# Performance work log

Measured on AMD Instinct MI355X. Metric: run time of the kernel, lower is better.

The kernel has to match this reference:

```python
import jax, jax.numpy as jnp
import numpy as np

EPS = 1e-5
RADIUS = 1.0

def bn(x, gamma, beta, axis=1):
    # inference-mode BatchNorm1d: running_mean=0, running_var=1
    shape = [1] * x.ndim
    shape[axis] = -1
    return x * (gamma / jnp.sqrt(1.0 + EPS)).reshape(shape) + beta.reshape(shape)

def pconv(x, w):
    # pointwise Conv1d (kernel_size=1): x [B,Cin,N], w [Cout,Cin]
    return jnp.einsum('oi,bin->bon', w, x)

def sq_dist(a, b):
    # a [B,N,3], b [B,S,3] -> squared pairwise distances [B,N,S]
    return (jnp.sum(a * a, -1)[:, :, None] + jnp.sum(b * b, -1)[:, None, :]
            - 2.0 * jnp.einsum('bnc,bsc->bns', a, b))

def index_points(points, idx):
    # points [B,S,...], idx [B,...] -> gathered [B, idx.shape[1:], ...]
    return jax.vmap(lambda p, i: p[i])(points, idx)

def fps(xyz, npoint):
    # farthest point sampling (deterministic start at index 0)
    B, N, _ = xyz.shape
    binds = jnp.arange(B)
    def step(carry, _):
        dist, far = carry
        c = xyz[binds, far]                                    # [B,3]
        d = jnp.sum((xyz - c[:, None, :]) ** 2, -1)            # [B,N]
        dist = jnp.minimum(dist, d)
        nxt = jnp.argmax(dist, -1).astype(jnp.int32)
        return (dist, nxt), far
    init = (jnp.full((B, N), 1e10, xyz.dtype), jnp.zeros((B,), jnp.int32))
    _, idx = jax.lax.scan(step, init, None, length=npoint)
    return jnp.transpose(idx)                                   # [B,npoint]

def query_ball(radius, nsample, xyz, new_xyz):
    # indices of first nsample points within radius of each center
    B, N, _ = xyz.shape
    S = new_xyz.shape[1]
    d2 = sq_dist(new_xyz, xyz)                                  # [B,S,N]
    gidx = jnp.broadcast_to(jnp.arange(N, dtype=jnp.int32), (B, S, N))
    gidx = jnp.where(d2 > radius * radius, N, gidx)
    gidx = jnp.sort(gidx, axis=-1)[:, :, :nsample]
    first = gidx[:, :, :1]
    gidx = jnp.where(gidx == N, first, gidx)
    return jnp.clip(gidx, 0, N - 1)

def sample_and_group(npoint, nsample, radius, xyz, points):
    fps_idx = fps(xyz, npoint)
    new_xyz = index_points(xyz, fps_idx)                        # [B,S,3]
    new_pts = index_points(points, fps_idx)                     # [B,S,D]
    idx = query_ball(radius, nsample, xyz, new_xyz)             # [B,S,K]
    grouped = index_points(points, idx)                         # [B,S,K,D]
    centered = grouped - new_pts[:, :, None, :]
    rep = jnp.broadcast_to(new_pts[:, :, None, :], centered.shape)
    return new_xyz, jnp.concatenate([centered, rep], axis=-1)   # [B,S,K,2D]

def local_op(x, w1, g1, b1, w2, g2, b2):
    # x [B,n,K,d]; shared pointwise MLP over channels then max over K
    h = jnp.einsum('oi,bnki->bnok', w1, x)
    h = jax.nn.relu(bn(h, g1, b1, axis=2))
    h = jnp.einsum('oi,bnik->bnok', w2, h)
    h = jax.nn.relu(bn(h, g2, b2, axis=2))
    return jnp.transpose(jnp.max(h, -1), (0, 2, 1))             # [B,out,n]

def feature_prop(xyz1, xyz2, points1, points2, w1, g1, b1, w2, g2, b2):
    # 3-NN inverse-distance interpolation of points2 onto xyz1, concat points1
    p1 = jnp.transpose(xyz1, (0, 2, 1))                         # [B,N,3]
    p2 = jnp.transpose(xyz2, (0, 2, 1))                         # [B,S,3]
    f2 = jnp.transpose(points2, (0, 2, 1))                      # [B,S,D2]
    negd, idx = jax.lax.top_k(-sq_dist(p1, p2), 3)              # [B,N,3]
    recip = 1.0 / (-negd + 1e-8)
    w = recip / jnp.sum(recip, -1, keepdims=True)
    interp = jnp.sum(index_points(f2, idx) * w[..., None], 2)   # [B,N,D2]
    new = jnp.concatenate([points1, jnp.transpose(interp, (0, 2, 1))], axis=1)
    new = jax.nn.relu(bn(pconv(new, w1), g1, b1))
    new = jax.nn.relu(bn(pconv(new, w2), g2, b2))
    return new


def setup_inputs() -> dict:
    key = jax.random.key(0)
    ks = iter(jax.random.split(key, 80))
    def W(*s):  return jax.random.normal(next(ks), s, jnp.float32) * 0.05
    def G(n):   return 1.0 + 0.1 * jax.random.normal(next(ks), (n,), jnp.float32)
    def Bt(n):  return 0.1 * jax.random.normal(next(ks), (n,), jnp.float32)
    inp = {"x": jax.random.uniform(next(ks), (4, 8192, 3), jnp.float32)}
    inp.update(w_emb1=W(64, 3), g_emb1=G(64), be_emb1=Bt(64),
               w_emb2=W(64, 64), g_emb2=G(64), be_emb2=Bt(64),
               l0_w1=W(128, 128), l0_g1=G(128), l0_b1=Bt(128),
               l0_w2=W(128, 128), l0_g2=G(128), l0_b2=Bt(128),
               l1_w1=W(256, 256), l1_g1=G(256), l1_b1=Bt(256),
               l1_w2=W(256, 256), l1_g2=G(256), l1_b2=Bt(256),
               f0_w1=W(256, 384), f0_g1=G(256), f0_b1=Bt(256),
               f0_w2=W(512, 256), f0_g2=G(512), f0_b2=Bt(512),
               f1_w1=W(512, 576), f1_g1=G(512), f1_b1=Bt(512),
               f1_w2=W(1024, 512), f1_g2=G(1024), f1_b2=Bt(1024),
               c1_w=W(512, 1024), c1_bias=Bt(512), c1_g=G(512), c1_beta=Bt(512),
               c2_w=W(128, 512), c2_bias=Bt(128), c2_g=G(128), c2_beta=Bt(128),
               out_w=W(8, 128), out_bias=Bt(8))
    return inp


def reference(x, w_emb1, g_emb1, be_emb1, w_emb2, g_emb2, be_emb2,
              l0_w1, l0_g1, l0_b1, l0_w2, l0_g2, l0_b2,
              l1_w1, l1_g1, l1_b1, l1_w2, l1_g2, l1_b2,
              f0_w1, f0_g1, f0_b1, f0_w2, f0_g2, f0_b2,
              f1_w1, f1_g1, f1_b1, f1_w2, f1_g2, f1_b2,
              c1_w, c1_bias, c1_g, c1_beta, c2_w, c2_bias, c2_g, c2_beta,
              out_w, out_bias):
    xyz = x                                                     # [B,N,3]
    h = jnp.transpose(x, (0, 2, 1))                             # [B,3,N]
    h = jax.nn.relu(bn(pconv(h, w_emb1), g_emb1, be_emb1))
    h = jax.nn.relu(bn(pconv(h, w_emb2), g_emb2, be_emb2))
    feats0 = h                                                  # [B,64,N]
    xyz1, g1f = sample_and_group(2048, 32, RADIUS, xyz, jnp.transpose(h, (0, 2, 1)))
    feats1 = local_op(g1f, l0_w1, l0_g1, l0_b1, l0_w2, l0_g2, l0_b2)   # [B,128,2048]
    xyz2, g2f = sample_and_group(1024, 32, RADIUS, xyz1, jnp.transpose(feats1, (0, 2, 1)))
    feats2 = local_op(g2f, l1_w1, l1_g1, l1_b1, l1_w2, l1_g2, l1_b2)   # [B,256,1024]
    h = feature_prop(jnp.transpose(xyz1, (0, 2, 1)), jnp.transpose(xyz2, (0, 2, 1)),
                     feats1, feats2, f0_w1, f0_g1, f0_b1, f0_w2, f0_g2, f0_b2)   # [B,512,2048]
    h = feature_prop(jnp.transpose(xyz, (0, 2, 1)), jnp.transpose(xyz1, (0, 2, 1)),
                     feats0, h, f1_w1, f1_g1, f1_b1, f1_w2, f1_g2, f1_b2)        # [B,1024,N]
    h = jax.nn.relu(bn(pconv(h, c1_w) + c1_bias[None, :, None], c1_g, c1_beta))
    h = jax.nn.relu(bn(pconv(h, c2_w) + c2_bias[None, :, None], c2_g, c2_beta))
    logits = pconv(h, out_w) + out_bias[None, :, None]
    return jnp.transpose(logits, (0, 2, 1))                     # [B,N,labels]
```

## Files before the change

### kernel.cpp

```cpp
#include <hip/hip_runtime.h>
#include <math.h>


static constexpr size_t O_FEATS0 = 0;
static constexpr size_t O_FEATS1 = 8388608;
static constexpr size_t O_FEATS2 = 12582912;
static constexpr size_t O_FP0OUT = 16777216;
static constexpr size_t O_XYZ1   = 33554432;
static constexpr size_t O_XYZ2   = 33652736;
static constexpr size_t O_FPS1   = 33701888;
static constexpr size_t O_FPS2   = 33734656;
static constexpr size_t O_BALL1  = 33751040;
static constexpr size_t O_BALL2  = 34799616;
static constexpr size_t O_NN0I   = 35323904;
static constexpr size_t O_NN0W   = 35422208;
static constexpr size_t O_NN1I   = 35520512;
static constexpr size_t O_NN1W   = 35913728;
static constexpr size_t O_REG0   = 36306944;
static constexpr size_t O_REG1   = 103415808;
static constexpr size_t WS_NEED  = 170524672;

typedef float v2f __attribute__((ext_vector_type(2)));

__device__ __forceinline__ unsigned long long u64max(unsigned long long a,
                                                     unsigned long long b) {
  return a > b ? a : b;
}
template <int CTRL>
__device__ __forceinline__ unsigned long long dpp_step(unsigned long long k) {
  const int lo = (int)(unsigned)k;
  const int hi = (int)(unsigned)(k >> 32);
  const int nlo = __builtin_amdgcn_update_dpp(lo, lo, CTRL, 0xf, 0xf, false);
  const int nhi = __builtin_amdgcn_update_dpp(hi, hi, CTRL, 0xf, 0xf, false);
  return ((unsigned long long)(unsigned)nhi << 32) | (unsigned)nlo;
}

template <int N, int NP, bool EMB>
__global__ __launch_bounds__(256, 1) void fps_kernel(
    const float* __restrict__ xyz, int* __restrict__ out,
    float* __restrict__ oxyz, const float* __restrict__ w1,
    const float* __restrict__ g1, const float* __restrict__ b1,
    const float* __restrict__ w2, const float* __restrict__ g2,
    const float* __restrict__ b2, float* __restrict__ femb) {
  #pragma clang fp contract(off)
  constexpr int PPT = N / 256;
  constexpr int PAIRS = PPT / 2;
  __shared__ float sx[N], sy[N], sz[N];
  __shared__ int sfar[NP];
  __shared__ unsigned long long skey[2][4];

  if constexpr (EMB) {
    if (blockIdx.x >= 4) {
      #pragma clang fp contract(fast)
      const int bid = blockIdx.x - 4;
      const int t = threadIdx.x;
      const int o = t & 63, pl = t >> 6;
      const int pt = bid * 4 + pl;
      const float x0 = xyz[(size_t)pt * 3 + 0];
      const float x1 = xyz[(size_t)pt * 3 + 1];
      const float x2 = xyz[(size_t)pt * 3 + 2];
      const float SQ = sqrtf(1.0f + 1e-5f);
      float v = w1[o * 3 + 0] * x0 + w1[o * 3 + 1] * x1 + w1[o * 3 + 2] * x2;
      v = fmaxf(v * (g1[o] / SQ) + b1[o], 0.0f);
      float* h = sx;
      h[pl * 64 + o] = v;
      __syncthreads();
      float acc = 0.0f;
      #pragma unroll 8
      for (int i = 0; i < 64; ++i) acc += w2[o * 64 + i] * h[pl * 64 + i];
      float y = fmaxf(acc * (g2[o] / SQ) + b2[o], 0.0f);
      femb[(size_t)pt * 64 + o] = y;
      return;
    }
  }

  const int b = blockIdx.x, t = threadIdx.x;
  const float* xb = xyz + (size_t)b * N * 3;
  for (int i = t; i < N; i += 256) {
    sx[i] = xb[i * 3 + 0];
    sy[i] = xb[i * 3 + 1];
    sz[i] = xb[i * 3 + 2];
  }
  __syncthreads();
  v2f px[PAIRS], py[PAIRS], pz[PAIRS], ds[PAIRS];
  #pragma unroll
  for (int k = 0; k < PAIRS; ++k) {
    const int g = t * PPT + 2 * k;
    px[k].x = sx[g]; px[k].y = sx[g + 1];
    py[k].x = sy[g]; py[k].y = sy[g + 1];
    pz[k].x = sz[g]; pz[k].y = sz[g + 1];
    ds[k].x = 1e10f; ds[k].y = 1e10f;
  }
  const int wid = t >> 6, lane = t & 63;
  int far = 0;
  float ccx = sx[0], ccy = sy[0], ccz = sz[0];
  for (int it = 0; it < NP; ++it) {
    if (t == 0) sfar[it] = far;
    v2f cx2, cy2, cz2;
    cx2.x = ccx; cx2.y = ccx;
    cy2.x = ccy; cy2.y = ccy;
    cz2.x = ccz; cz2.y = ccz;
    #pragma unroll
    for (int k = 0; k < PAIRS; ++k) {
      const v2f dx = px[k] - cx2;
      const v2f dy = py[k] - cy2;
      const v2f dz = pz[k] - cz2;
      const v2f d = dx * dx + dy * dy + dz * dz;
      v2f nd;
      nd.x = fminf(ds[k].x, d.x);
      nd.y = fminf(ds[k].y, d.y);
      ds[k] = nd;
    }
    v2f tv[PAIRS / 2];
    #pragma unroll
    for (int k = 0; k < PAIRS / 2; ++k) {
      tv[k].x = fmaxf(ds[k].x, ds[k + PAIRS / 2].x);
      tv[k].y = fmaxf(ds[k].y, ds[k + PAIRS / 2].y);
    }
    #pragma unroll
    for (int w = PAIRS / 4; w >= 1; w >>= 1) {
      #pragma unroll
      for (int k = 0; k < w; ++k) {
        tv[k].x = fmaxf(tv[k].x, tv[k + w].x);
        tv[k].y = fmaxf(tv[k].y, tv[k + w].y);
      }
    }
    const float bv = fmaxf(tv[0].x, tv[0].y);
    unsigned mask = 0u;
    #pragma unroll
    for (int k = 0; k < PAIRS; ++k) {
      mask |= (ds[k].x == bv) ? (1u << (2 * k)) : 0u;
      mask |= (ds[k].y == bv) ? (1u << (2 * k + 1)) : 0u;
    }
    const int bjl = __builtin_ctz(mask);
    unsigned long long bk =
        ((unsigned long long)__float_as_uint(bv) << 32) |
        (unsigned long long)(unsigned)(~(unsigned)(t * PPT + bjl));
    bk = u64max(bk, dpp_step<0x111>(bk));
    bk = u64max(bk, dpp_step<0x112>(bk));
    bk = u64max(bk, dpp_step<0x114>(bk));
    bk = u64max(bk, dpp_step<0x118>(bk));
    bk = u64max(bk, dpp_step<0x142>(bk));
    bk = u64max(bk, dpp_step<0x143>(bk));
    const int p = it & 1;
    if (lane == 63) skey[p][wid] = bk;
    __syncthreads();
    unsigned long long wk = skey[p][0];
    #pragma unroll
    for (int q = 1; q < 4; ++q) {
      const unsigned long long k2 = skey[p][q];
      wk = (k2 > wk) ? k2 : wk;
    }
    far = (int)(~(unsigned)wk);
    ccx = sx[far]; ccy = sy[far]; ccz = sz[far];
  }
  __syncthreads();
  for (int i = t; i < NP; i += 256) {
    const int n = sfar[i];
    out[(size_t)b * NP + i] = n;
    oxyz[((size_t)b * NP + i) * 3 + 0] = sx[n];
    oxyz[((size_t)b * NP + i) * 3 + 1] = sy[n];
    oxyz[((size_t)b * NP + i) * 3 + 2] = sz[n];
  }
}

__global__ __launch_bounds__(256) void ballnn_kernel(
    const float* __restrict__ cloud, const float* __restrict__ ctr,
    int* __restrict__ ballOut, int sbits, int N, int nBallBlk,
    const float* __restrict__ txyz, const float* __restrict__ sxyz,
    int* __restrict__ oi, float* __restrict__ ow, int s1bits, int S2) {
  __shared__ int lists[4][32];
  __shared__ float ss[6144];
  const int t = threadIdx.x;
  if ((int)blockIdx.x < nBallBlk) {
    const int lane = t & 63, wid = t >> 6;
    const int wg = blockIdx.x * 4 + wid;
    const int b = wg >> sbits;
    const float cx = ctr[(size_t)wg * 3 + 0];
    const float cy = ctr[(size_t)wg * 3 + 1];
    const float cz = ctr[(size_t)wg * 3 + 2];
    const float an = __fadd_rn(__fadd_rn(__fmul_rn(cx, cx), __fmul_rn(cy, cy)),
                               __fmul_rn(cz, cz));
    int fill = 0;
    for (int ch = 0; ch < (N >> 6) && fill < 32; ++ch) {
      const int n = ch * 64 + lane;
      const float bx = cloud[((size_t)b * N + n) * 3 + 0];
      const float by = cloud[((size_t)b * N + n) * 3 + 1];
      const float bz = cloud[((size_t)b * N + n) * 3 + 2];
      const float bb = __fadd_rn(
          __fadd_rn(__fmul_rn(bx, bx), __fmul_rn(by, by)), __fmul_rn(bz, bz));
      const float dot = __fadd_rn(
          __fadd_rn(__fmul_rn(cx, bx), __fmul_rn(cy, by)), __fmul_rn(cz, bz));
      const float d2 = __fsub_rn(__fadd_rn(an, bb), __fmul_rn(2.0f, dot));
      const bool q = (d2 <= 1.0f);
      const unsigned long long mask = __ballot(q);
      if (q) {
        const int pos = fill + __popcll(mask & ((1ull << lane) - 1ull));
        if (pos < 32) lists[wid][pos] = n;
      }
      fill += (int)__popcll(mask);
    }
    __syncthreads();
    if (lane < 32) {
      int v = lists[wid][0];
      if (lane < fill) v = lists[wid][lane];
      ballOut[(size_t)wg * 32 + lane] = v;
    }
    return;
  }
  const int row = (blockIdx.x - nBallBlk) * 256 + t;
  const int b = row >> s1bits;
  for (int i = t; i < S2 * 3; i += 256) ss[i] = sxyz[(size_t)b * S2 * 3 + i];
  __syncthreads();
  const float ax = txyz[(size_t)row * 3 + 0];
  const float ay = txyz[(size_t)row * 3 + 1];
  const float az = txyz[(size_t)row * 3 + 2];
  const float an = __fadd_rn(__fadd_rn(__fmul_rn(ax, ax), __fmul_rn(ay, ay)),
                             __fmul_rn(az, az));
  float d0 = 3.4e38f, d1 = 3.4e38f, d2v = 3.4e38f;
  int i0 = 0, i1 = 0, i2 = 0;
  for (int j = 0; j < S2; ++j) {
    const float bx = ss[j * 3 + 0], by = ss[j * 3 + 1], bz = ss[j * 3 + 2];
    const float bb = __fadd_rn(__fadd_rn(__fmul_rn(bx, bx), __fmul_rn(by, by)),
                               __fmul_rn(bz, bz));
    const float dot = __fadd_rn(__fadd_rn(__fmul_rn(ax, bx), __fmul_rn(ay, by)),
                                __fmul_rn(az, bz));
    const float dd = __fsub_rn(__fadd_rn(an, bb), __fmul_rn(2.0f, dot));
    if (dd < d0) {
      d2v = d1; i2 = i1; d1 = d0; i1 = i0; d0 = dd; i0 = j;
    } else if (dd < d1) {
      d2v = d1; i2 = i1; d1 = dd; i1 = j;
    } else if (dd < d2v) {
      d2v = dd; i2 = j;
    }
  }
  const float r0 = 1.0f / (d0 + 1e-8f);
  const float r1 = 1.0f / (d1 + 1e-8f);
  const float r2 = 1.0f / (d2v + 1e-8f);
  const float sum = __fadd_rn(__fadd_rn(r0, r1), r2);
  oi[(size_t)row * 3 + 0] = i0;
  oi[(size_t)row * 3 + 1] = i1;
  oi[(size_t)row * 3 + 2] = i2;
  ow[(size_t)row * 3 + 0] = r0 / sum;
  ow[(size_t)row * 3 + 1] = r1 / sum;
  ow[(size_t)row * 3 + 2] = r2 / sum;
}

#define CMAP(c) ((((c) >> 3) * 12) + ((c) & 7))

__global__ __launch_bounds__(256) void conv_gather_kernel(
    const float* __restrict__ f, const int* __restrict__ ball,
    const int* __restrict__ fps, int g0, int Cf, int sbits, int Npts,
    const float* __restrict__ W, float* __restrict__ Y, int O,
    const float* __restrict__ gamma, const float* __restrict__ beta) {
  const int C = Cf * 2;
  __shared__ float Xs[16][188];
  __shared__ float Ws[16][188];
  const int t = threadIdx.x;
  const size_t m0 = (size_t)blockIdx.x * 128;
  const int o0 = blockIdx.y * 128;
  const int r0 = t >> 2;
  const int cq0 = (t & 3) * 4;
  const int mq = t & 15, nq = t >> 4;
  const int ca = CMAP(r0), cb = CMAP(r0 + 64);
  const int mA = (int)m0 + r0, mB = (int)m0 + r0 + 64;
  const int glA = g0 + (mA >> 5), glB = g0 + (mB >> 5);
  const int srcA = ball[(size_t)glA * 32 + (mA & 31)];
  const int srcB = ball[(size_t)glB * 32 + (mB & 31)];
  const int ctrA = fps[glA], ctrB = fps[glB];
  const float* fbA = f + (size_t)(glA >> sbits) * Npts * Cf;
  const float* fbB = f + (size_t)(glB >> sbits) * Npts * Cf;
  v2f acc[8][4];
  #pragma unroll
  for (int i = 0; i < 8; ++i)
    #pragma unroll
    for (int j = 0; j < 4; ++j) acc[i][j] = (v2f){0.0f, 0.0f};

  for (int kk = 0; kk < C; kk += 16) {
    const int col = kk + cq0;
    const bool lo = col < Cf;
    const int col2 = lo ? col : col - Cf;
    float4 xa, xb;
    {
      const float4 c4 = *(const float4*)(fbA + (size_t)ctrA * Cf + col2);
      if (lo) {
        const float4 s4 = *(const float4*)(fbA + (size_t)srcA * Cf + col);
        xa = make_float4(s4.x - c4.x, s4.y - c4.y, s4.z - c4.z, s4.w - c4.w);
      } else {
        xa = c4;
      }
    }
    {
      const float4 c4 = *(const float4*)(fbB + (size_t)ctrB * Cf + col2);
      if (lo) {
        const float4 s4 = *(const float4*)(fbB + (size_t)srcB * Cf + col);
        xb = make_float4(s4.x - c4.x, s4.y - c4.y, s4.z - c4.z, s4.w - c4.w);
      } else {
        xb = c4;
      }
    }
    const float4 wa = *(const float4*)(W + (size_t)(o0 + r0) * C + kk + cq0);
    const float4 wb =
        *(const float4*)(W + (size_t)(o0 + r0 + 64) * C + kk + cq0);
    __syncthreads();
    Xs[cq0 + 0][ca] = xa.x; Xs[cq0 + 1][ca] = xa.y;
    Xs[cq0 + 2][ca] = xa.z; Xs[cq0 + 3][ca] = xa.w;
    Xs[cq0 + 0][cb] = xb.x; Xs[cq0 + 1][cb] = xb.y;
    Xs[cq0 + 2][cb] = xb.z; Xs[cq0 + 3][cb] = xb.w;
    Ws[cq0 + 0][ca] = wa.x; Ws[cq0 + 1][ca] = wa.y;
    Ws[cq0 + 2][ca] = wa.z; Ws[cq0 + 3][ca] = wa.w;
    Ws[cq0 + 0][cb] = wb.x; Ws[cq0 + 1][cb] = wb.y;
    Ws[cq0 + 2][cb] = wb.z; Ws[cq0 + 3][cb] = wb.w;
    __syncthreads();
    #pragma unroll
    for (int k = 0; k < 16; ++k) {
      const float4 a0 = *(const float4*)&Xs[k][mq * 12];
      const float4 a1 = *(const float4*)&Xs[k][mq * 12 + 4];
      const float4 b0 = *(const float4*)&Ws[k][nq * 12];
      const float4 b1 = *(const float4*)&Ws[k][nq * 12 + 4];
      const float am[8] = {a0.x, a0.y, a0.z, a0.w, a1.x, a1.y, a1.z, a1.w};
      v2f bv[4];
      bv[0] = (v2f){b0.x, b0.y};
      bv[1] = (v2f){b0.z, b0.w};
      bv[2] = (v2f){b1.x, b1.y};
      bv[3] = (v2f){b1.z, b1.w};
      #pragma unroll
      for (int i = 0; i < 8; ++i) {
        const v2f as = (v2f){am[i], am[i]};
        #pragma unroll
        for (int j = 0; j < 4; ++j) acc[i][j] += as * bv[j];
      }
    }
  }

  const float SQ = sqrtf(1.0f + 1e-5f);
  float s[8], sh[8];
  #pragma unroll
  for (int j = 0; j < 8; ++j) {
    const int o = o0 + nq * 8 + j;
    s[j] = gamma[o] / SQ;
    sh[j] = beta[o];
  }
  #pragma unroll
  for (int i = 0; i < 8; ++i) {
    float y[8];
    #pragma unroll
    for (int j = 0; j < 4; ++j) {
      y[2 * j] = fmaxf(acc[i][j].x * s[2 * j] + sh[2 * j], 0.0f);
      y[2 * j + 1] = fmaxf(acc[i][j].y * s[2 * j + 1] + sh[2 * j + 1], 0.0f);
    }
    const size_t off = (m0 + mq * 8 + i) * O + o0 + nq * 8;
    *(float4*)(Y + off) = make_float4(y[0], y[1], y[2], y[3]);
    *(float4*)(Y + off + 4) = make_float4(y[4], y[5], y[6], y[7]);
  }
}

__global__ __launch_bounds__(256) void conv2sm_kernel(
    const float* __restrict__ X, const float* __restrict__ W,
    float* __restrict__ F, int C, int O, const float* __restrict__ gamma,
    const float* __restrict__ beta) {
  __shared__ float Xs[16][188];
  __shared__ float Ws[16][188];
  const int t = threadIdx.x;
  const size_t m0 = (size_t)blockIdx.x * 128;
  const int o0 = blockIdx.y * 128;
  const int r0 = t >> 2;
  const int cq0 = (t & 3) * 4;
  const int mq = t & 15, nq = t >> 4;
  const int ca = CMAP(r0), cb = CMAP(r0 + 64);
  v2f acc[8][4];
  #pragma unroll
  for (int i = 0; i < 8; ++i)
    #pragma unroll
    for (int j = 0; j < 4; ++j) acc[i][j] = (v2f){0.0f, 0.0f};

  for (int kk = 0; kk < C; kk += 16) {
    const float4 xa = *(const float4*)(X + (m0 + r0) * C + kk + cq0);
    const float4 xb = *(const float4*)(X + (m0 + r0 + 64) * C + kk + cq0);
    const float4 wa = *(const float4*)(W + (size_t)(o0 + r0) * C + kk + cq0);
    const float4 wb =
        *(const float4*)(W + (size_t)(o0 + r0 + 64) * C + kk + cq0);
    __syncthreads();
    Xs[cq0 + 0][ca] = xa.x; Xs[cq0 + 1][ca] = xa.y;
    Xs[cq0 + 2][ca] = xa.z; Xs[cq0 + 3][ca] = xa.w;
    Xs[cq0 + 0][cb] = xb.x; Xs[cq0 + 1][cb] = xb.y;
    Xs[cq0 + 2][cb] = xb.z; Xs[cq0 + 3][cb] = xb.w;
    Ws[cq0 + 0][ca] = wa.x; Ws[cq0 + 1][ca] = wa.y;
    Ws[cq0 + 2][ca] = wa.z; Ws[cq0 + 3][ca] = wa.w;
    Ws[cq0 + 0][cb] = wb.x; Ws[cq0 + 1][cb] = wb.y;
    Ws[cq0 + 2][cb] = wb.z; Ws[cq0 + 3][cb] = wb.w;
    __syncthreads();
    #pragma unroll
    for (int k = 0; k < 16; ++k) {
      const float4 a0 = *(const float4*)&Xs[k][mq * 12];
      const float4 a1 = *(const float4*)&Xs[k][mq * 12 + 4];
      const float4 b0 = *(const float4*)&Ws[k][nq * 12];
      const float4 b1 = *(const float4*)&Ws[k][nq * 12 + 4];
      const float am[8] = {a0.x, a0.y, a0.z, a0.w, a1.x, a1.y, a1.z, a1.w};
      v2f bv[4];
      bv[0] = (v2f){b0.x, b0.y};
      bv[1] = (v2f){b0.z, b0.w};
      bv[2] = (v2f){b1.x, b1.y};
      bv[3] = (v2f){b1.z, b1.w};
      #pragma unroll
      for (int i = 0; i < 8; ++i) {
        const v2f as = (v2f){am[i], am[i]};
        #pragma unroll
        for (int j = 0; j < 4; ++j) acc[i][j] += as * bv[j];
      }
    }
  }

  const float SQ = sqrtf(1.0f + 1e-5f);
  float s[8], sh[8];
  #pragma unroll
  for (int j = 0; j < 8; ++j) {
    const int o = o0 + nq * 8 + j;
    s[j] = gamma[o] / SQ;
    sh[j] = beta[o];
  }
  float colmax[8];
  #pragma unroll
  for (int j = 0; j < 8; ++j) colmax[j] = -3.4e38f;
  #pragma unroll
  for (int i = 0; i < 8; ++i) {
    #pragma unroll
    for (int j = 0; j < 4; ++j) {
      const float va = fmaxf(acc[i][j].x * s[2 * j] + sh[2 * j], 0.0f);
      const float vb = fmaxf(acc[i][j].y * s[2 * j + 1] + sh[2 * j + 1], 0.0f);
      colmax[2 * j] = fmaxf(colmax[2 * j], va);
      colmax[2 * j + 1] = fmaxf(colmax[2 * j + 1], vb);
    }
  }
  __syncthreads();
  float* smax = &Xs[0][0];
  #pragma unroll
  for (int j = 0; j < 8; ++j) smax[mq * 132 + nq * 8 + j] = colmax[j];
  __syncthreads();
  #pragma unroll
  for (int q = 0; q < 2; ++q) {
    const int idx = t + q * 256;
    const int g = idx >> 7;
    const int col = idx & 127;
    const float m =
        fmaxf(fmaxf(smax[(4 * g + 0) * 132 + col], smax[(4 * g + 1) * 132 + col]),
              fmaxf(smax[(4 * g + 2) * 132 + col], smax[(4 * g + 3) * 132 + col]));
    F[(size_t)(blockIdx.x * 4 + g) * O + o0 + col] = m;
  }
}

__global__ __launch_bounds__(256) void conv_kernel(
    const float* __restrict__ X, const float* __restrict__ W,
    float* __restrict__ Y, int C, int O, const float* __restrict__ gamma,
    const float* __restrict__ beta, const float* __restrict__ bias, int relu) {
  __shared__ float Xs[16][188];
  __shared__ float Ws[16][188];
  const int t = threadIdx.x;
  const size_t m0 = (size_t)blockIdx.x * 128;
  const int o0 = blockIdx.y * 128;
  const int r0 = t >> 2;
  const int cq0 = (t & 3) * 4;
  const int mq = t & 15, nq = t >> 4;
  const int ca = CMAP(r0), cb = CMAP(r0 + 64);
  v2f acc[8][4];
  #pragma unroll
  for (int i = 0; i < 8; ++i)
    #pragma unroll
    for (int j = 0; j < 4; ++j) acc[i][j] = (v2f){0.0f, 0.0f};

  for (int kk = 0; kk < C; kk += 16) {
    const float4 xa = *(const float4*)(X + (m0 + r0) * C + kk + cq0);
    const float4 xb = *(const float4*)(X + (m0 + r0 + 64) * C + kk + cq0);
    const float4 wa = *(const float4*)(W + (size_t)(o0 + r0) * C + kk + cq0);
    const float4 wb =
        *(const float4*)(W + (size_t)(o0 + r0 + 64) * C + kk + cq0);
    __syncthreads();
    Xs[cq0 + 0][ca] = xa.x; Xs[cq0 + 1][ca] = xa.y;
    Xs[cq0 + 2][ca] = xa.z; Xs[cq0 + 3][ca] = xa.w;
    Xs[cq0 + 0][cb] = xb.x; Xs[cq0 + 1][cb] = xb.y;
    Xs[cq0 + 2][cb] = xb.z; Xs[cq0 + 3][cb] = xb.w;
    Ws[cq0 + 0][ca] = wa.x; Ws[cq0 + 1][ca] = wa.y;
    Ws[cq0 + 2][ca] = wa.z; Ws[cq0 + 3][ca] = wa.w;
    Ws[cq0 + 0][cb] = wb.x; Ws[cq0 + 1][cb] = wb.y;
    Ws[cq0 + 2][cb] = wb.z; Ws[cq0 + 3][cb] = wb.w;
    __syncthreads();
    #pragma unroll
    for (int k = 0; k < 16; ++k) {
      const float4 a0 = *(const float4*)&Xs[k][mq * 12];
      const float4 a1 = *(const float4*)&Xs[k][mq * 12 + 4];
      const float4 b0 = *(const float4*)&Ws[k][nq * 12];
      const float4 b1 = *(const float4*)&Ws[k][nq * 12 + 4];
      const float am[8] = {a0.x, a0.y, a0.z, a0.w, a1.x, a1.y, a1.z, a1.w};
      v2f bv[4];
      bv[0] = (v2f){b0.x, b0.y};
      bv[1] = (v2f){b0.z, b0.w};
      bv[2] = (v2f){b1.x, b1.y};
      bv[3] = (v2f){b1.z, b1.w};
      #pragma unroll
      for (int i = 0; i < 8; ++i) {
        const v2f as = (v2f){am[i], am[i]};
        #pragma unroll
        for (int j = 0; j < 4; ++j) acc[i][j] += as * bv[j];
      }
    }
  }

  const float SQ = sqrtf(1.0f + 1e-5f);
  float s[8], sh[8];
  #pragma unroll
  for (int j = 0; j < 8; ++j) {
    const int o = o0 + nq * 8 + j;
    const float sc = gamma ? (gamma[o] / SQ) : 1.0f;
    float bb = beta ? beta[o] : 0.0f;
    if (bias) bb = bb + bias[o] * sc;
    s[j] = sc; sh[j] = bb;
  }
  #pragma unroll
  for (int i = 0; i < 8; ++i) {
    float y[8];
    #pragma unroll
    for (int j = 0; j < 4; ++j) {
      float va = acc[i][j].x * s[2 * j] + sh[2 * j];
      float vb = acc[i][j].y * s[2 * j + 1] + sh[2 * j + 1];
      y[2 * j] = relu ? fmaxf(va, 0.0f) : va;
      y[2 * j + 1] = relu ? fmaxf(vb, 0.0f) : vb;
    }
    const size_t off = (m0 + mq * 8 + i) * O + o0 + nq * 8;
    *(float4*)(Y + off) = make_float4(y[0], y[1], y[2], y[3]);
    *(float4*)(Y + off + 4) = make_float4(y[4], y[5], y[6], y[7]);
  }
}

__global__ __launch_bounds__(256) void interp_kernel(
    float* __restrict__ dst, int CT, int c0, const float* __restrict__ src,
    const int* __restrict__ idx, const float* __restrict__ w, int csbits,
    int s1bits, int S2) {
  const int id = blockIdx.x * 256 + threadIdx.x;
  const int row = id >> csbits;
  const int c4 = (id & ((1 << csbits) - 1)) * 4;
  const int Cs = 4 << csbits;
  const int b = row >> s1bits;
  const int j0 = idx[(size_t)row * 3 + 0];
  const int j1 = idx[(size_t)row * 3 + 1];
  const int j2 = idx[(size_t)row * 3 + 2];
  const float w0 = w[(size_t)row * 3 + 0];
  const float w1 = w[(size_t)row * 3 + 1];
  const float w2 = w[(size_t)row * 3 + 2];
  const float4 f0 = *(const float4*)(src + ((size_t)b * S2 + j0) * Cs + c4);
  const float4 f1 = *(const float4*)(src + ((size_t)b * S2 + j1) * Cs + c4);
  const float4 f2 = *(const float4*)(src + ((size_t)b * S2 + j2) * Cs + c4);
  float4 v;
  v.x = f0.x * w0 + f1.x * w1 + f2.x * w2;
  v.y = f0.y * w0 + f1.y * w1 + f2.y * w2;
  v.z = f0.z * w0 + f1.z * w1 + f2.z * w2;
  v.w = f0.w * w0 + f1.w * w1 + f2.w * w2;
  *(float4*)(dst + (size_t)row * CT + c0 + c4) = v;
}

__global__ __launch_bounds__(256) void copycols_kernel(
    float* __restrict__ dst, int CT, int c0, const float* __restrict__ src,
    int csbits) {
  const int id = blockIdx.x * 256 + threadIdx.x;
  const int row = id >> csbits;
  const int c4 = (id & ((1 << csbits) - 1)) * 4;
  const int Cs = 4 << csbits;
  const float4 v = *(const float4*)(src + (size_t)row * Cs + c4);
  *(float4*)(dst + (size_t)row * CT + c0 + c4) = v;
}

__global__ __launch_bounds__(256) void outfinal_kernel(
    const float* __restrict__ X, const float* __restrict__ Wt,
    const float* __restrict__ bias, float* __restrict__ out) {
  __shared__ float Xs[32][132];
  const int t = threadIdx.x;
  const int p0 = blockIdx.x * 32;
  #pragma unroll
  for (int q = 0; q < 4; ++q) {
    const int id = t + q * 256;
    const int r = id >> 5, c4 = (id & 31) * 4;
    const float4 v = *(const float4*)(X + (size_t)(p0 + r) * 128 + c4);
    Xs[r][c4 + 0] = v.x; Xs[r][c4 + 1] = v.y;
    Xs[r][c4 + 2] = v.z; Xs[r][c4 + 3] = v.w;
  }
  __syncthreads();
  const int p = t >> 3, o = t & 7;
  float acc = 0.0f;
  #pragma unroll 8
  for (int i = 0; i < 128; ++i) acc += Wt[o * 128 + i] * Xs[p][i];
  out[(size_t)(p0 + p) * 8 + o] = acc + bias[o];
}

extern "C" void kernel_launch(void* const* d_in, const int* in_sizes, int n_in,
                              void* d_out, int out_size, void* d_ws,
                              size_t ws_size, hipStream_t stream) {
  const float* x       = (const float*)d_in[0];
  const float* w_emb1  = (const float*)d_in[1];
  const float* g_emb1  = (const float*)d_in[2];
  const float* be_emb1 = (const float*)d_in[3];
  const float* w_emb2  = (const float*)d_in[4];
  const float* g_emb2  = (const float*)d_in[5];
  const float* be_emb2 = (const float*)d_in[6];
  const float* l0_w1 = (const float*)d_in[7];
  const float* l0_g1 = (const float*)d_in[8];
  const float* l0_b1 = (const float*)d_in[9];
  const float* l0_w2 = (const float*)d_in[10];
  const float* l0_g2 = (const float*)d_in[11];
  const float* l0_b2 = (const float*)d_in[12];
  const float* l1_w1 = (const float*)d_in[13];
  const float* l1_g1 = (const float*)d_in[14];
  const float* l1_b1 = (const float*)d_in[15];
  const float* l1_w2 = (const float*)d_in[16];
  const float* l1_g2 = (const float*)d_in[17];
  const float* l1_b2 = (const float*)d_in[18];
  const float* f0_w1 = (const float*)d_in[19];
  const float* f0_g1 = (const float*)d_in[20];
  const float* f0_b1 = (const float*)d_in[21];
  const float* f0_w2 = (const float*)d_in[22];
  const float* f0_g2 = (const float*)d_in[23];
  const float* f0_b2 = (const float*)d_in[24];
  const float* f1_w1 = (const float*)d_in[25];
  const float* f1_g1 = (const float*)d_in[26];
  const float* f1_b1 = (const float*)d_in[27];
  const float* f1_w2 = (const float*)d_in[28];
  const float* f1_g2 = (const float*)d_in[29];
  const float* f1_b2 = (const float*)d_in[30];
  const float* c1_w    = (const float*)d_in[31];
  const float* c1_bias = (const float*)d_in[32];
  const float* c1_g    = (const float*)d_in[33];
  const float* c1_beta = (const float*)d_in[34];
  const float* c2_w    = (const float*)d_in[35];
  const float* c2_bias = (const float*)d_in[36];
  const float* c2_g    = (const float*)d_in[37];
  const float* c2_beta = (const float*)d_in[38];
  const float* out_w    = (const float*)d_in[39];
  const float* out_bias = (const float*)d_in[40];

  if (ws_size < WS_NEED) return;

  char* ws = (char*)d_ws;
  float* feats0 = (float*)(ws + O_FEATS0);
  float* feats1 = (float*)(ws + O_FEATS1);
  float* feats2 = (float*)(ws + O_FEATS2);
  float* fp0out = (float*)(ws + O_FP0OUT);
  float* xyz1   = (float*)(ws + O_XYZ1);
  float* xyz2   = (float*)(ws + O_XYZ2);
  int*   fps1   = (int*)(ws + O_FPS1);
  int*   fps2   = (int*)(ws + O_FPS2);
  int*   ball1  = (int*)(ws + O_BALL1);
  int*   ball2  = (int*)(ws + O_BALL2);
  int*   nn0i   = (int*)(ws + O_NN0I);
  float* nn0w   = (float*)(ws + O_NN0W);
  int*   nn1i   = (int*)(ws + O_NN1I);
  float* nn1w   = (float*)(ws + O_NN1W);
  float* REG0   = (float*)(ws + O_REG0);
  float* REG1   = (float*)(ws + O_REG1);
  float* outp   = (float*)d_out;
  hipStream_t s = stream;

  fps_kernel<8192, 2048, true><<<4 + 8192, 256, 0, s>>>(
      x, fps1, xyz1, w_emb1, g_emb1, be_emb1, w_emb2, g_emb2, be_emb2, feats0);

  ballnn_kernel<<<2048 + 128, 256, 0, s>>>(x, xyz1, ball1, 11, 8192, 2048,
                                           x, xyz1, nn1i, nn1w, 13, 2048);

  for (int c = 0; c < 2; ++c) {
    conv_gather_kernel<<<dim3(1024, 1), 256, 0, s>>>(
        feats0, ball1, fps1, c * 4096, 64, 11, 8192, l0_w1, REG1, 128, l0_g1,
        l0_b1);
    conv2sm_kernel<<<dim3(1024, 1), 256, 0, s>>>(
        REG1, l0_w2, feats1 + (size_t)c * 4096 * 128, 128, 128, l0_g2, l0_b2);
  }

  fps_kernel<2048, 1024, false><<<4, 256, 0, s>>>(
      xyz1, fps2, xyz2, nullptr, nullptr, nullptr, nullptr, nullptr, nullptr,
      nullptr);

  ballnn_kernel<<<1024 + 32, 256, 0, s>>>(xyz1, xyz2, ball2, 10, 2048, 1024,
                                          xyz1, xyz2, nn0i, nn0w, 11, 1024);

  for (int c = 0; c < 2; ++c) {
    conv_gather_kernel<<<dim3(512, 2), 256, 0, s>>>(
        feats1, ball2, fps2, c * 2048, 128, 10, 2048, l1_w1, REG1, 256, l1_g1,
        l1_b1);
    conv2sm_kernel<<<dim3(512, 2), 256, 0, s>>>(
        REG1, l1_w2, feats2 + (size_t)c * 2048 * 256, 256, 256, l1_g2, l1_b2);
  }

  copycols_kernel<<<1024, 256, 0, s>>>(REG0, 384, 0, feats1, 5);
  interp_kernel<<<2048, 256, 0, s>>>(REG0, 384, 128, feats2, nn0i, nn0w, 6, 11,
                                     1024);
  conv_kernel<<<dim3(64, 2), 256, 0, s>>>(REG0, f0_w1, REG1, 384, 256, f0_g1,
                                          f0_b1, nullptr, 1);
  conv_kernel<<<dim3(64, 4), 256, 0, s>>>(REG1, f0_w2, fp0out, 256, 512, f0_g2,
                                          f0_b2, nullptr, 1);

  for (int b = 0; b < 4; b += 2) {
    copycols_kernel<<<1024, 256, 0, s>>>(REG0, 576, 0,
                                         feats0 + (size_t)b * 8192 * 64, 4);
    interp_kernel<<<8192, 256, 0, s>>>(REG0, 576, 64,
                                       fp0out + (size_t)b * 2048 * 512,
                                       nn1i + (size_t)b * 8192 * 3,
                                       nn1w + (size_t)b * 8192 * 3, 7, 13,
                                       2048);
    conv_kernel<<<dim3(128, 4), 256, 0, s>>>(REG0, f1_w1, REG1, 576, 512,
                                             f1_g1, f1_b1, nullptr, 1);
    conv_kernel<<<dim3(128, 8), 256, 0, s>>>(REG1, f1_w2, REG0, 512, 1024,
                                             f1_g2, f1_b2, nullptr, 1);
    conv_kernel<<<dim3(128, 4), 256, 0, s>>>(REG0, c1_w, REG1, 1024, 512,
                                             c1_g, c1_beta, c1_bias, 1);
    conv_kernel<<<dim3(128, 1), 256, 0, s>>>(REG1, c2_w, REG0, 512, 128,
                                             c2_g, c2_beta, c2_bias, 1);
    outfinal_kernel<<<512, 256, 0, s>>>(REG0, out_w, out_bias,
                                        outp + (size_t)b * 8192 * 8);
  }
}
```

Measured before the change: 4.907 ms.

## Fuse second FPS into ball-query launch and merge copy+interp kernels

Moves the second-level farthest point sampling (4 serial blocks) into the first ball-query/NN kernel as extra blocks, so the long sequential FPS overlaps with the ball-query and three-NN work rather than running as its own launch between the conv stages. It also merges the column copy and interpolation kernels into a single concat_interp kernel, removing launches. The fused kernel uses launch_bounds(256,1) and a shared buffer sized for FPS, which may reduce occupancy for the ball/NN blocks.

```diff
diff --git a/kernel.cpp b/kernel.cpp
--- a/kernel.cpp
+++ b/kernel.cpp
@@ -35,46 +35,14 @@
   return ((unsigned long long)(unsigned)nhi << 32) | (unsigned)nlo;
 }
 
-template <int N, int NP, bool EMB>
-__global__ __launch_bounds__(256, 1) void fps_kernel(
-    const float* __restrict__ xyz, int* __restrict__ out,
-    float* __restrict__ oxyz, const float* __restrict__ w1,
-    const float* __restrict__ g1, const float* __restrict__ b1,
-    const float* __restrict__ w2, const float* __restrict__ g2,
-    const float* __restrict__ b2, float* __restrict__ femb) {
+template <int N, int NP>
+__device__ void fps_core(const float* __restrict__ xyz, int* __restrict__ out,
+                         float* __restrict__ oxyz, float* sx, float* sy,
+                         float* sz, int* sfar, unsigned long long* skey,
+                         int b, int t) {
   #pragma clang fp contract(off)
   constexpr int PPT = N / 256;
   constexpr int PAIRS = PPT / 2;
-  __shared__ float sx[N], sy[N], sz[N];
-  __shared__ int sfar[NP];
-  __shared__ unsigned long long skey[2][4];
-
-  if constexpr (EMB) {
-    if (blockIdx.x >= 4) {
-      #pragma clang fp contract(fast)
-      const int bid = blockIdx.x - 4;
-      const int t = threadIdx.x;
-      const int o = t & 63, pl = t >> 6;
-      const int pt = bid * 4 + pl;
-      const float x0 = xyz[(size_t)pt * 3 + 0];
-      const float x1 = xyz[(size_t)pt * 3 + 1];
-      const float x2 = xyz[(size_t)pt * 3 + 2];
-      const float SQ = sqrtf(1.0f + 1e-5f);
-      float v = w1[o * 3 + 0] * x0 + w1[o * 3 + 1] * x1 + w1[o * 3 + 2] * x2;
-      v = fmaxf(v * (g1[o] / SQ) + b1[o], 0.0f);
-      float* h = sx;
-      h[pl * 64 + o] = v;
-      __syncthreads();
-      float acc = 0.0f;
-      #pragma unroll 8
-      for (int i = 0; i < 64; ++i) acc += w2[o * 64 + i] * h[pl * 64 + i];
-      float y = fmaxf(acc * (g2[o] / SQ) + b2[o], 0.0f);
-      femb[(size_t)pt * 64 + o] = y;
-      return;
-    }
-  }
-
-  const int b = blockIdx.x, t = threadIdx.x;
   const float* xb = xyz + (size_t)b * N * 3;
   for (int i = t; i < N; i += 256) {
     sx[i] = xb[i * 3 + 0];
@@ -143,12 +111,12 @@
     bk = u64max(bk, dpp_step<0x142>(bk));
     bk = u64max(bk, dpp_step<0x143>(bk));
     const int p = it & 1;
-    if (lane == 63) skey[p][wid] = bk;
-    __syncthreads();
-    unsigned long long wk = skey[p][0];
+    if (lane == 63) skey[p * 4 + wid] = bk;
+    __syncthreads();
+    unsigned long long wk = skey[p * 4 + 0];
     #pragma unroll
     for (int q = 1; q < 4; ++q) {
-      const unsigned long long k2 = skey[p][q];
+      const unsigned long long k2 = skey[p * 4 + q];
       wk = (k2 > wk) ? k2 : wk;
     }
     far = (int)(~(unsigned)wk);
@@ -162,6 +130,136 @@
     oxyz[((size_t)b * NP + i) * 3 + 1] = sy[n];
     oxyz[((size_t)b * NP + i) * 3 + 2] = sz[n];
   }
+}
+
+template <int N, int NP>
+__global__ __launch_bounds__(256, 1) void fps_emb_kernel(
+    const float* __restrict__ xyz, int* __restrict__ out,
+    float* __restrict__ oxyz, const float* __restrict__ w1,
+    const float* __restrict__ g1, const float* __restrict__ b1,
+    const float* __restrict__ w2, const float* __restrict__ g2,
+    const float* __restrict__ b2, float* __restrict__ femb) {
+  __shared__ float sx[N], sy[N], sz[N];
+  __shared__ int sfar[NP];
+  __shared__ unsigned long long skey[8];
+  if (blockIdx.x >= 4) {
+    const int bid = blockIdx.x - 4;
+    const int t = threadIdx.x;
+    const int o = t & 63, pl = t >> 6;
+    const int pt = bid * 4 + pl;
+    const float x0 = xyz[(size_t)pt * 3 + 0];
+    const float x1 = xyz[(size_t)pt * 3 + 1];
+    const float x2 = xyz[(size_t)pt * 3 + 2];
+    const float SQ = sqrtf(1.0f + 1e-5f);
+    float v = w1[o * 3 + 0] * x0 + w1[o * 3 + 1] * x1 + w1[o * 3 + 2] * x2;
+    v = fmaxf(v * (g1[o] / SQ) + b1[o], 0.0f);
+    float* h = sx;
+    h[pl * 64 + o] = v;
+    __syncthreads();
+    float acc = 0.0f;
+    #pragma unroll 8
+    for (int i = 0; i < 64; ++i) acc += w2[o * 64 + i] * h[pl * 64 + i];
+    float y = fmaxf(acc * (g2[o] / SQ) + b2[o], 0.0f);
+    femb[(size_t)pt * 64 + o] = y;
+    return;
+  }
+  fps_core<N, NP>(xyz, out, oxyz, sx, sy, sz, sfar, skey, blockIdx.x,
+                  threadIdx.x);
+}
+
+__global__ __launch_bounds__(256, 1) void ballnnfps_kernel(
+    const float* __restrict__ cloud, const float* __restrict__ ctr,
+    int* __restrict__ ballOut, int sbits, int N, int nBallBlk,
+    const float* __restrict__ txyz, const float* __restrict__ sxyz,
+    int* __restrict__ oi, float* __restrict__ ow, int s1bits, int S2,
+    const float* __restrict__ fxyz, int* __restrict__ fout,
+    float* __restrict__ foxyz) {
+  __shared__ __align__(16) char smem[28800];
+  const int t = threadIdx.x;
+  if ((int)blockIdx.x < 4) {
+    unsigned long long* skey = (unsigned long long*)smem;
+    int* sfar = (int*)(smem + 64);
+    float* sx = (float*)(smem + 64 + 4096);
+    float* sy = sx + 2048;
+    float* sz = sy + 2048;
+    fps_core<2048, 1024>(fxyz, fout, foxyz, sx, sy, sz, sfar, skey,
+                         blockIdx.x, t);
+    return;
+  }
+  if ((int)blockIdx.x < 4 + nBallBlk) {
+    int* lists = (int*)smem;
+    const int lane = t & 63, wid = t >> 6;
+    const int wg = (blockIdx.x - 4) * 4 + wid;
+    const int b = wg >> sbits;
+    const float cx = ctr[(size_t)wg * 3 + 0];
+    const float cy = ctr[(size_t)wg * 3 + 1];
+    const float cz = ctr[(size_t)wg * 3 + 2];
+    const float an = __fadd_rn(__fadd_rn(__fmul_rn(cx, cx), __fmul_rn(cy, cy)),
+                               __fmul_rn(cz, cz));
+    int fill = 0;
+    for (int ch = 0; ch < (N >> 6) && fill < 32; ++ch) {
+      const int n = ch * 64 + lane;
+      const float bx = cloud[((size_t)b * N + n) * 3 + 0];
+      const float by = cloud[((size_t)b * N + n) * 3 + 1];
+      const float bz = cloud[((size_t)b * N + n) * 3 + 2];
+      const float bb = __fadd_rn(
+          __fadd_rn(__fmul_rn(bx, bx), __fmul_rn(by, by)), __fmul_rn(bz, bz));
+      const float dot = __fadd_rn(
+          __fadd_rn(__fmul_rn(cx, bx), __fmul_rn(cy, by)), __fmul_rn(cz, bz));
+      const float d2 = __fsub_rn(__fadd_rn(an, bb), __fmul_rn(2.0f, dot));
+      const bool q = (d2 <= 1.0f);
+      const unsigned long long mask = __ballot(q);
+      if (q) {
+        const int pos = fill + __popcll(mask & ((1ull << lane) - 1ull));
+        if (pos < 32) lists[wid * 32 + pos] = n;
+      }
+      fill += (int)__popcll(mask);
+    }
+    __syncthreads();
+    if (lane < 32) {
+      int v = lists[wid * 32 + 0];
+      if (lane < fill) v = lists[wid * 32 + lane];
+      ballOut[(size_t)wg * 32 + lane] = v;
+    }
+    return;
+  }
+  float* ss = (float*)smem;
+  const int row = (blockIdx.x - 4 - nBallBlk) * 256 + t;
+  const int b = row >> s1bits;
+  for (int i = t; i < S2 * 3; i += 256) ss[i] = sxyz[(size_t)b * S2 * 3 + i];
+  __syncthreads();
+  const float ax = txyz[(size_t)row * 3 + 0];
+  const float ay = txyz[(size_t)row * 3 + 1];
+  const float az = txyz[(size_t)row * 3 + 2];
+  const float an = __fadd_rn(__fadd_rn(__fmul_rn(ax, ax), __fmul_rn(ay, ay)),
+                             __fmul_rn(az, az));
+  float d0 = 3.4e38f, d1 = 3.4e38f, d2v = 3.4e38f;
+  int i0 = 0, i1 = 0, i2 = 0;
+  for (int j = 0; j < S2; ++j) {
+    const float bx = ss[j * 3 + 0], by = ss[j * 3 + 1], bz = ss[j * 3 + 2];
+    const float bb = __fadd_rn(__fadd_rn(__fmul_rn(bx, bx), __fmul_rn(by, by)),
+                               __fmul_rn(bz, bz));
+    const float dot = __fadd_rn(__fadd_rn(__fmul_rn(ax, bx), __fmul_rn(ay, by)),
+                                __fmul_rn(az, bz));
+    const float dd = __fsub_rn(__fadd_rn(an, bb), __fmul_rn(2.0f, dot));
+    if (dd < d0) {
+      d2v = d1; i2 = i1; d1 = d0; i1 = i0; d0 = dd; i0 = j;
+    } else if (dd < d1) {
+      d2v = d1; i2 = i1; d1 = dd; i1 = j;
+    } else if (dd < d2v) {
+      d2v = dd; i2 = j;
+    }
+  }
+  const float r0 = 1.0f / (d0 + 1e-8f);
+  const float r1 = 1.0f / (d1 + 1e-8f);
+  const float r2 = 1.0f / (d2v + 1e-8f);
+  const float sum = __fadd_rn(__fadd_rn(r0, r1), r2);
+  oi[(size_t)row * 3 + 0] = i0;
+  oi[(size_t)row * 3 + 1] = i1;
+  oi[(size_t)row * 3 + 2] = i2;
+  ow[(size_t)row * 3 + 0] = r0 / sum;
+  ow[(size_t)row * 3 + 1] = r1 / sum;
+  ow[(size_t)row * 3 + 2] = r2 / sum;
 }
 
 __global__ __launch_bounds__(256) void ballnn_kernel(
@@ -531,41 +629,37 @@
   }
 }
 
-__global__ __launch_bounds__(256) void interp_kernel(
-    float* __restrict__ dst, int CT, int c0, const float* __restrict__ src,
-    const int* __restrict__ idx, const float* __restrict__ w, int csbits,
-    int s1bits, int S2) {
+template <int CT, int C0, int CS2>
+__global__ __launch_bounds__(256) void concat_interp_kernel(
+    float* __restrict__ dst, const float* __restrict__ srcA,
+    const float* __restrict__ srcB, const int* __restrict__ idx,
+    const float* __restrict__ w, int s1bits, int S2) {
   const int id = blockIdx.x * 256 + threadIdx.x;
-  const int row = id >> csbits;
-  const int c4 = (id & ((1 << csbits) - 1)) * 4;
-  const int Cs = 4 << csbits;
-  const int b = row >> s1bits;
-  const int j0 = idx[(size_t)row * 3 + 0];
-  const int j1 = idx[(size_t)row * 3 + 1];
-  const int j2 = idx[(size_t)row * 3 + 2];
-  const float w0 = w[(size_t)row * 3 + 0];
-  const float w1 = w[(size_t)row * 3 + 1];
-  const float w2 = w[(size_t)row * 3 + 2];
-  const float4 f0 = *(const float4*)(src + ((size_t)b * S2 + j0) * Cs + c4);
-  const float4 f1 = *(const float4*)(src + ((size_t)b * S2 + j1) * Cs + c4);
-  const float4 f2 = *(const float4*)(src + ((size_t)b * S2 + j2) * Cs + c4);
-  float4 v;
-  v.x = f0.x * w0 + f1.x * w1 + f2.x * w2;
-  v.y = f0.y * w0 + f1.y * w1 + f2.y * w2;
-  v.z = f0.z * w0 + f1.z * w1 + f2.z * w2;
-  v.w = f0.w * w0 + f1.w * w1 + f2.w * w2;
-  *(float4*)(dst + (size_t)row * CT + c0 + c4) = v;
-}
-
-__global__ __launch_bounds__(256) void copycols_kernel(
-    float* __restrict__ dst, int CT, int c0, const float* __restrict__ src,
-    int csbits) {
-  const int id = blockIdx.x * 256 + threadIdx.x;
-  const int row = id >> csbits;
-  const int c4 = (id & ((1 << csbits) - 1)) * 4;
-  const int Cs = 4 << csbits;
-  const float4 v = *(const float4*)(src + (size_t)row * Cs + c4);
-  *(float4*)(dst + (size_t)row * CT + c0 + c4) = v;
+  constexpr int CPR = CT / 4;
+  const int row = id / CPR;
+  const int c4 = (id - row * CPR) * 4;
+  if (c4 < C0) {
+    const float4 v = *(const float4*)(srcA + (size_t)row * C0 + c4);
+    *(float4*)(dst + (size_t)row * CT + c4) = v;
+  } else {
+    const int b = row >> s1bits;
+    const int cc = c4 - C0;
+    const int j0 = idx[(size_t)row * 3 + 0];
+    const int j1 = idx[(size_t)row * 3 + 1];
+    const int j2 = idx[(size_t)row * 3 + 2];
+    const float w0 = w[(size_t)row * 3 + 0];
+    const float w1 = w[(size_t)row * 3 + 1];
+    const float w2 = w[(size_t)row * 3 + 2];
+    const float4 f0 = *(const float4*)(srcB + ((size_t)b * S2 + j0) * CS2 + cc);
+    const float4 f1 = *(const float4*)(srcB + ((size_t)b * S2 + j1) * CS2 + cc);
+    const float4 f2 = *(const float4*)(srcB + ((size_t)b * S2 + j2) * CS2 + cc);
+    float4 v;
+    v.x = f0.x * w0 + f1.x * w1 + f2.x * w2;
+    v.y = f0.y * w0 + f1.y * w1 + f2.y * w2;
+    v.z = f0.z * w0 + f1.z * w1 + f2.z * w2;
+    v.w = f0.w * w0 + f1.w * w1 + f2.w * w2;
+    *(float4*)(dst + (size_t)row * CT + c4) = v;
+  }
 }
 
 __global__ __launch_bounds__(256) void outfinal_kernel(
@@ -657,11 +751,12 @@
   float* outp   = (float*)d_out;
   hipStream_t s = stream;
 
-  fps_kernel<8192, 2048, true><<<4 + 8192, 256, 0, s>>>(
+  fps_emb_kernel<8192, 2048><<<4 + 8192, 256, 0, s>>>(
       x, fps1, xyz1, w_emb1, g_emb1, be_emb1, w_emb2, g_emb2, be_emb2, feats0);
 
-  ballnn_kernel<<<2048 + 128, 256, 0, s>>>(x, xyz1, ball1, 11, 8192, 2048,
-                                           x, xyz1, nn1i, nn1w, 13, 2048);
+  ballnnfps_kernel<<<4 + 2048 + 128, 256, 0, s>>>(
+      x, xyz1, ball1, 11, 8192, 2048, x, xyz1, nn1i, nn1w, 13, 2048,
+      xyz1, fps2, xyz2);
 
   for (int c = 0; c < 2; ++c) {
     conv_gather_kernel<<<dim3(1024, 1), 256, 0, s>>>(
@@ -671,10 +766,6 @@
         REG1, l0_w2, feats1 + (size_t)c * 4096 * 128, 128, 128, l0_g2, l0_b2);
   }
 
-  fps_kernel<2048, 1024, false><<<4, 256, 0, s>>>(
-      xyz1, fps2, xyz2, nullptr, nullptr, nullptr, nullptr, nullptr, nullptr,
-      nullptr);
-
   ballnn_kernel<<<1024 + 32, 256, 0, s>>>(xyz1, xyz2, ball2, 10, 2048, 1024,
                                           xyz1, xyz2, nn0i, nn0w, 11, 1024);
 
@@ -686,22 +777,17 @@
         REG1, l1_w2, feats2 + (size_t)c * 2048 * 256, 256, 256, l1_g2, l1_b2);
   }
 
-  copycols_kernel<<<1024, 256, 0, s>>>(REG0, 384, 0, feats1, 5);
-  interp_kernel<<<2048, 256, 0, s>>>(REG0, 384, 128, feats2, nn0i, nn0w, 6, 11,
-                                     1024);
+  concat_interp_kernel<384, 128, 256><<<3072, 256, 0, s>>>(
+      REG0, feats1, feats2, nn0i, nn0w, 11, 1024);
   conv_kernel<<<dim3(64, 2), 256, 0, s>>>(REG0, f0_w1, REG1, 384, 256, f0_g1,
                                           f0_b1, nullptr, 1);
   conv_kernel<<<dim3(64, 4), 256, 0, s>>>(REG1, f0_w2, fp0out, 256, 512, f0_g2,
                                           f0_b2, nullptr, 1);
 
   for (int b = 0; b < 4; b += 2) {
-    copycols_kernel<<<1024, 256, 0, s>>>(REG0, 576, 0,
-                                         feats0 + (size_t)b * 8192 * 64, 4);
-    interp_kernel<<<8192, 256, 0, s>>>(REG0, 576, 64,
-                                       fp0out + (size_t)b * 2048 * 512,
-                                       nn1i + (size_t)b * 8192 * 3,
-                                       nn1w + (size_t)b * 8192 * 3, 7, 13,
-                                       2048);
+    concat_interp_kernel<576, 64, 512><<<9216, 256, 0, s>>>(
+        REG0, feats0 + (size_t)b * 8192 * 64, fp0out + (size_t)b * 2048 * 512,
+        nn1i + (size_t)b * 8192 * 3, nn1w + (size_t)b * 8192 * 3, 13, 2048);
     conv_kernel<<<dim3(128, 4), 256, 0, s>>>(REG0, f1_w1, REG1, 576, 512,
                                              f1_g1, f1_b1, nullptr, 1);
     conv_kernel<<<dim3(128, 8), 256, 0, s>>>(REG1, f1_w2, REG0, 512, 1024,
```

Result: faster. 4.618 ms (-5.9%).
